# Optimization experiments

Measured on AMD Instinct MI355X. Metric: run time of the kernel, lower is better.

## Reference

```python
import jax, jax.numpy as jnp
import numpy as np

EPS = 1e-5

def layer_norm(x, alpha, beta):
    mean = jnp.mean(x, axis=-1, keepdims=True)
    var = jnp.mean(jnp.square(x - mean), axis=-1, keepdims=True)
    return alpha * ((x - mean) / jnp.sqrt(var + EPS)) + beta

def setup_inputs() -> dict:
    key = jax.random.key(0)
    B, S, D, H = 4, 2048, 1024, 16
    Dff = 4 * D
    ks = jax.random.split(key, 8)
    inp = {
        "x": jax.random.normal(ks[0], (B, S, D), jnp.float32),
        "attention_mask": jnp.ones((B, S), jnp.int32),
        "ln1_alpha": jnp.ones((D,), jnp.float32),
        "ln1_beta": jnp.zeros((D,), jnp.float32),
        "ln2_alpha": jnp.ones((D,), jnp.float32),
        "ln2_beta": jnp.zeros((D,), jnp.float32),
        "Wq": jax.random.normal(ks[1], (D, D), jnp.float32) * 0.05,
        "Wk": jax.random.normal(ks[2], (D, D), jnp.float32) * 0.05,
        "Wv": jax.random.normal(ks[3], (D, D), jnp.float32) * 0.05,
        "Wo": jax.random.normal(ks[4], (D, D), jnp.float32) * 0.05,
        "W1": jax.random.normal(ks[5], (D, Dff), jnp.float32) * 0.02,
        "b1": jnp.zeros((Dff,), jnp.float32),
        "W2": jax.random.normal(ks[6], (Dff, D), jnp.float32) * 0.02,
        "b2": jnp.zeros((D,), jnp.float32),
    }
    return inp

def reference(x, attention_mask, ln1_alpha, ln1_beta, ln2_alpha, ln2_beta,
              Wq, Wk, Wv, Wo, W1, b1, W2, b2):
    B, S, D = x.shape
    H = 16
    dh = D // H

    # LN1 + self-attention
    y = layer_norm(x, ln1_alpha, ln1_beta)
    Q = (y @ Wq).reshape(B, S, H, dh).transpose(0, 2, 1, 3)  # [B,H,S,dh]
    K = (y @ Wk).reshape(B, S, H, dh).transpose(0, 2, 1, 3)
    V = (y @ Wv).reshape(B, S, H, dh).transpose(0, 2, 1, 3)

    scores = jnp.einsum("bhqd,bhkd->bhqk", Q, K) / jnp.sqrt(jnp.float32(dh))
    causal = jnp.tril(jnp.ones((S, S), jnp.float32))  # [S,S]
    tmask = attention_mask.astype(jnp.float32)  # [B,S]
    amask = causal[None, None, :, :] * tmask[:, None, None, :] * tmask[:, None, :, None]
    scores = jnp.where(amask > 0, scores, jnp.float32(-1e30))
    attn = jax.nn.softmax(scores, axis=-1)
    # dropout omitted (deterministic inference)
    ctx = jnp.einsum("bhqk,bhkd->bhqd", attn, V)
    ctx = ctx.transpose(0, 2, 1, 3).reshape(B, S, D)
    x = x + ctx @ Wo

    # LN2 + GELU FFN
    y = layer_norm(x, ln2_alpha, ln2_beta)
    h = jax.nn.gelu(y @ W1 + b1, approximate=False)
    x = x + (h @ W2 + b2)
    return x
```

## Files before the change

### kernel.cpp

```cpp
#include <hip/hip_runtime.h>
#include <math.h>

typedef unsigned short u16;
typedef unsigned int u32;
typedef __attribute__((ext_vector_type(4))) unsigned short u16x4;
typedef __attribute__((ext_vector_type(8))) short bf16x8;
typedef __attribute__((ext_vector_type(4))) float f32x4;

#define B_ 4
#define S_ 2048
#define D_ 1024
#define H_ 16
#define NT (B_*S_)
#define DFF 4096

static __device__ __forceinline__ float bf2f(u16 u) {
    return __uint_as_float(((u32)u) << 16);
}
static __device__ __forceinline__ u16 f2bf(float f) {
    u32 u = __float_as_uint(f);
    u32 r = (u + 0x7fffu + ((u >> 16) & 1u)) >> 16;
    return (u16)r;
}
static __device__ __forceinline__ void gload_lds16(const void* g, void* l) {
    __builtin_amdgcn_global_load_lds(
        (const __attribute__((address_space(1))) void*)g,
        (__attribute__((address_space(3))) void*)l, 16, 0, 0);
}

__global__ void transpose_f2b4(const float* __restrict__ s0, const float* __restrict__ s1,
                               const float* __restrict__ s2, const float* __restrict__ s3,
                               u16* __restrict__ d0, u16* __restrict__ d1,
                               u16* __restrict__ d2, u16* __restrict__ d3,
                               int R, int C) {
    const float* in = s0; u16* out = d0;
    if (blockIdx.z == 1) { in = s1; out = d1; }
    else if (blockIdx.z == 2) { in = s2; out = d2; }
    else if (blockIdx.z == 3) { in = s3; out = d3; }
    __shared__ float t[32][33];
    int c0 = blockIdx.x * 32, r0 = blockIdx.y * 32;
    int x = threadIdx.x, y = threadIdx.y;
    #pragma unroll
    for (int i = 0; i < 4; i++)
        t[y + i*8][x] = in[(long)(r0 + y + i*8) * C + c0 + x];
    __syncthreads();
    #pragma unroll
    for (int i = 0; i < 4; i++)
        out[(long)(c0 + y + i*8) * R + r0 + x] = f2bf(t[x][y + i*8]);
}

__global__ void transpose_f2b(const float* __restrict__ in, u16* __restrict__ out,
                              int R, int C) {
    __shared__ float t[32][33];
    int c0 = blockIdx.x * 32, r0 = blockIdx.y * 32;
    int x = threadIdx.x, y = threadIdx.y;
    #pragma unroll
    for (int i = 0; i < 4; i++)
        t[y + i*8][x] = in[(long)(r0 + y + i*8) * C + c0 + x];
    __syncthreads();
    #pragma unroll
    for (int i = 0; i < 4; i++)
        out[(long)(c0 + y + i*8) * R + r0 + x] = f2bf(t[x][y + i*8]);
}

__global__ void transpose_v(const u16* __restrict__ V, u16* __restrict__ Vt) {
    __shared__ u16 t[32][33];
    int z = blockIdx.z; int b = z >> 4, h = z & 15;
    int s0 = blockIdx.x * 32, d0 = blockIdx.y * 32;
    int x = threadIdx.x, y = threadIdx.y;
    const u16* in = V + ((long)b * S_ + s0) * D_ + h * 64 + d0;
    #pragma unroll
    for (int i = 0; i < 4; i++)
        t[y + i*8][x] = in[(long)(y + i*8) * D_ + x];
    __syncthreads();
    u16* out = Vt + ((long)z * 64 + d0) * S_ + s0;
    #pragma unroll
    for (int i = 0; i < 4; i++)
        out[(long)(y + i*8) * S_ + x] = t[x][y + i*8];
}

__global__ __launch_bounds__(256) void ln_kernel(
    const float* __restrict__ X, const float* __restrict__ alpha,
    const float* __restrict__ beta, u16* __restrict__ Y) {
    int row = blockIdx.x, tid = threadIdx.x;
    float4 xv = ((const float4*)(X + (long)row * D_))[tid];
    float v[4] = {xv.x, xv.y, xv.z, xv.w};
    float s = 0.f, ss = 0.f;
    #pragma unroll
    for (int i = 0; i < 4; i++) { s += v[i]; ss += v[i]*v[i]; }
    #pragma unroll
    for (int off = 32; off >= 1; off >>= 1) {
        s += __shfl_xor(s, off);
        ss += __shfl_xor(ss, off);
    }
    __shared__ float red[8];
    __shared__ float stats[2];
    int w = tid >> 6;
    if ((tid & 63) == 0) { red[w] = s; red[4 + w] = ss; }
    __syncthreads();
    if (tid == 0) {
        float S = red[0] + red[1] + red[2] + red[3];
        float SS = red[4] + red[5] + red[6] + red[7];
        float mean = S * (1.f / D_);
        float var = SS * (1.f / D_) - mean * mean;
        stats[0] = mean; stats[1] = rsqrtf(var + 1e-5f);
    }
    __syncthreads();
    float mean = stats[0], rstd = stats[1];
    float4 av = ((const float4*)alpha)[tid];
    float4 bv = ((const float4*)beta)[tid];
    u16x4 o;
    o[0] = f2bf((v[0] - mean) * rstd * av.x + bv.x);
    o[1] = f2bf((v[1] - mean) * rstd * av.y + bv.y);
    o[2] = f2bf((v[2] - mean) * rstd * av.z + bv.z);
    o[3] = f2bf((v[3] - mean) * rstd * av.w + bv.w);
    *(u16x4*)(Y + (long)row * D_ + tid * 4) = o;
}

#define BM 128
#define BN 128
#define BK 64

__global__ __launch_bounds__(256, 3) void gemm_bt(
    const u16* __restrict__ A,
    const u16* __restrict__ Bt0, const u16* __restrict__ Bt1, const u16* __restrict__ Bt2,
    void* __restrict__ C0, void* __restrict__ C1, void* __restrict__ C2,
    int M, int N, int K, int mode,
    const float* __restrict__ bias, const float* __restrict__ resid) {
    const u16* Bt = Bt0; void* C = C0;
    if (blockIdx.z == 1) { Bt = Bt1; C = C1; }
    else if (blockIdx.z == 2) { Bt = Bt2; C = C2; }

    __shared__ __align__(16) u16 Asm[BM * BK];
    __shared__ __align__(16) u16 Bsm[BN * BK];

    int tid = threadIdx.x;
    int lane = tid & 63, wave = tid >> 6;
    int l15 = lane & 15, quad = lane >> 4;
    int wm = wave & 1, wn = wave >> 1;
    long tm0 = (long)blockIdx.y * BM, tn0 = (long)blockIdx.x * BN;

    int srow = lane >> 3;
    int scol = (lane & 7) * 8;

    f32x4 acc[4][4] = {};

    for (int k0 = 0; k0 < K; k0 += BK) {
        __syncthreads();
        #pragma unroll
        for (int c = 0; c < 4; c++) {
            int chunk = wave * 4 + c;
            int row = chunk * 8 + srow;
            gload_lds16(&A[(tm0 + row) * (long)K + k0 + scol], &Asm[chunk * 512]);
            gload_lds16(&Bt[(tn0 + row) * (long)K + k0 + scol], &Bsm[chunk * 512]);
        }
        __syncthreads();
        #pragma unroll
        for (int ks = 0; ks < 2; ks++) {
            bf16x8 af[4], bfm[4];
            #pragma unroll
            for (int mt = 0; mt < 4; mt++)
                af[mt] = *(const bf16x8*)&Asm[(wm*64 + mt*16 + l15) * BK + ks*32 + quad*8];
            #pragma unroll
            for (int nt = 0; nt < 4; nt++)
                bfm[nt] = *(const bf16x8*)&Bsm[(wn*64 + nt*16 + l15) * BK + ks*32 + quad*8];
            #pragma unroll
            for (int mt = 0; mt < 4; mt++)
                #pragma unroll
                for (int nt = 0; nt < 4; nt++)
                    acc[mt][nt] = __builtin_amdgcn_mfma_f32_16x16x32_bf16(
                        af[mt], bfm[nt], acc[mt][nt], 0, 0, 0);
        }
    }

    #pragma unroll
    for (int mt = 0; mt < 4; mt++) {
        #pragma unroll
        for (int nt = 0; nt < 4; nt++) {
            #pragma unroll
            for (int i = 0; i < 4; i++) {
                long r = tm0 + wm*64 + mt*16 + quad*4 + i;
                long cn = tn0 + wn*64 + nt*16 + l15;
                long idx = r * N + cn;
                float val = acc[mt][nt][i];
                if (mode == 0) {
                    ((u16*)C)[idx] = f2bf(val);
                } else if (mode == 1) {
                    ((float*)C)[idx] = val + resid[idx];
                } else if (mode == 2) {
                    val += bias[cn];
                    val = 0.5f * val * (1.0f + erff(val * 0.70710678118654752f));
                    ((u16*)C)[idx] = f2bf(val);
                } else {
                    ((float*)C)[idx] = val + bias[cn] + resid[idx];
                }
            }
        }
    }
}

#define LDP 72

__global__ __launch_bounds__(256, 2) void attn_kernel(
    const u16* __restrict__ Q, const u16* __restrict__ Kg, const u16* __restrict__ Vt,
    const int* __restrict__ mask, u16* __restrict__ O) {
    __shared__ __align__(16) u16 Psm[4][32 * LDP];
    int tid = threadIdx.x;
    int lane = tid & 63, wave = tid >> 6;
    int l15 = lane & 15, quad = lane >> 4;
    int bh = blockIdx.x; int b = bh >> 4, h = bh & 15;
    int y = blockIdx.y;
    long tokBase = (long)b * S_;
    const float SCL = 0.125f * 1.4426950408889634f;
    const float MMAX = 20.0f;

    const bf16x8 ones = {16256,16256,16256,16256,16256,16256,16256,16256};
    u16* Pw = Psm[wave];
    const int* mb = mask + b * S_;

    int t;
    if (wave == 0)      t = y;
    else if (wave == 1) t = 63 - y;
    else if (wave == 2) t = 31 - y;
    else                t = 32 + y;
    int q0 = t * 32;

    bf16x8 aq[2][2];
    #pragma unroll
    for (int mt = 0; mt < 2; mt++) {
        const u16* qptr = Q + (tokBase + q0 + mt*16 + l15) * D_ + h * 64;
        aq[mt][0] = *(const bf16x8*)(qptr + quad * 8);
        aq[mt][1] = *(const bf16x8*)(qptr + 32 + quad * 8);
    }

    f32x4 o[2][4] = {};
    f32x4 lacc[2] = {};
    int ktiles = t / 2 + 1;

    for (int kt = 0; kt < ktiles; kt++) {
        int k0 = kt * 64;
        bf16x8 kb[4][2], vb[4][2];
        #pragma unroll
        for (int nt = 0; nt < 4; nt++) {
            const u16* kp = Kg + (tokBase + k0 + nt*16 + l15) * D_ + h * 64;
            kb[nt][0] = *(const bf16x8*)(kp + quad * 8);
            kb[nt][1] = *(const bf16x8*)(kp + 32 + quad * 8);
        }
        #pragma unroll
        for (int d = 0; d < 4; d++) {
            const u16* vp = Vt + ((long)bh * 64 + d*16 + l15) * S_ + k0;
            vb[d][0] = *(const bf16x8*)(vp + quad * 8);
            vb[d][1] = *(const bf16x8*)(vp + 32 + quad * 8);
        }

        f32x4 s[2][4] = {};
        #pragma unroll
        for (int nt = 0; nt < 4; nt++) {
            s[0][nt] = __builtin_amdgcn_mfma_f32_16x16x32_bf16(aq[0][0], kb[nt][0], s[0][nt], 0,0,0);
            s[0][nt] = __builtin_amdgcn_mfma_f32_16x16x32_bf16(aq[0][1], kb[nt][1], s[0][nt], 0,0,0);
            s[1][nt] = __builtin_amdgcn_mfma_f32_16x16x32_bf16(aq[1][0], kb[nt][0], s[1][nt], 0,0,0);
            s[1][nt] = __builtin_amdgcn_mfma_f32_16x16x32_bf16(aq[1][1], kb[nt][1], s[1][nt], 0,0,0);
        }

        int mk = 0;
        #pragma unroll
        for (int nt = 0; nt < 4; nt++)
            if (mb[k0 + nt*16 + l15] != 0) mk |= (1 << nt);

        #pragma unroll
        for (int mt = 0; mt < 2; mt++) {
            #pragma unroll
            for (int i = 0; i < 4; i++) {
                int qq = q0 + mt*16 + quad*4 + i;
                #pragma unroll
                for (int nt = 0; nt < 4; nt++) {
                    int kc = k0 + nt*16 + l15;
                    float p = exp2f(fmaf(s[mt][nt][i], SCL, -MMAX));
                    p = (kc <= qq && ((mk >> nt) & 1)) ? p : 0.f;
                    Pw[(mt*16 + quad*4 + i) * LDP + nt*16 + l15] = f2bf(p);
                }
            }
        }
        asm volatile("s_waitcnt lgkmcnt(0)" ::: "memory");

        #pragma unroll
        for (int hv = 0; hv < 2; hv++) {
            bf16x8 ap0 = *(const bf16x8*)&Pw[l15 * LDP + hv*32 + quad*8];
            bf16x8 ap1 = *(const bf16x8*)&Pw[(16 + l15) * LDP + hv*32 + quad*8];
            #pragma unroll
            for (int d = 0; d < 4; d++) {
                o[0][d] = __builtin_amdgcn_mfma_f32_16x16x32_bf16(ap0, vb[d][hv], o[0][d], 0,0,0);
                o[1][d] = __builtin_amdgcn_mfma_f32_16x16x32_bf16(ap1, vb[d][hv], o[1][d], 0,0,0);
            }
            lacc[0] = __builtin_amdgcn_mfma_f32_16x16x32_bf16(ap0, ones, lacc[0], 0,0,0);
            lacc[1] = __builtin_amdgcn_mfma_f32_16x16x32_bf16(ap1, ones, lacc[1], 0,0,0);
        }
    }

    #pragma unroll
    for (int mt = 0; mt < 2; mt++) {
        #pragma unroll
        for (int i = 0; i < 4; i++) {
            float inv = 1.f / lacc[mt][i];
            long r = tokBase + q0 + mt*16 + quad*4 + i;
            #pragma unroll
            for (int d = 0; d < 4; d++)
                O[r * D_ + h*64 + d*16 + l15] = f2bf(o[mt][d][i] * inv);
        }
    }
}

extern "C" void kernel_launch(void* const* d_in, const int* in_sizes, int n_in,
                              void* d_out, int out_size, void* d_ws, size_t ws_size,
                              hipStream_t stream) {
    const float* x    = (const float*)d_in[0];
    const int*   am   = (const int*)d_in[1];
    const float* ln1a = (const float*)d_in[2];
    const float* ln1b = (const float*)d_in[3];
    const float* ln2a = (const float*)d_in[4];
    const float* ln2b = (const float*)d_in[5];
    const float* wq   = (const float*)d_in[6];
    const float* wk   = (const float*)d_in[7];
    const float* wv   = (const float*)d_in[8];
    const float* wo   = (const float*)d_in[9];
    const float* w1   = (const float*)d_in[10];
    const float* b1   = (const float*)d_in[11];
    const float* w2   = (const float*)d_in[12];
    const float* b2   = (const float*)d_in[13];
    float* out = (float*)d_out;

    char* ws = (char*)d_ws;
    const size_t MB16 = (size_t)16 * 1024 * 1024;
    u16* y1      = (u16*)(ws + 0 * MB16);
    u16* q       = (u16*)(ws + 1 * MB16);
    u16* k       = (u16*)(ws + 2 * MB16);
    u16* v       = (u16*)(ws + 3 * MB16);
    u16* wqt     = (u16*)(ws + 4 * MB16 + 0 * (size_t)D_ * D_ * 2);
    u16* wkt     = (u16*)(ws + 4 * MB16 + 1 * (size_t)D_ * D_ * 2);
    u16* wvt     = (u16*)(ws + 4 * MB16 + 2 * (size_t)D_ * D_ * 2);
    u16* wot     = (u16*)(ws + 4 * MB16 + 3 * (size_t)D_ * D_ * 2);
    u16* y2      = y1;
    u16* w1t     = q;
    u16* w2t     = q + (size_t)D_ * DFF;
    u16* h_full  = k;
    u16* ctx     = v;
    u16*   vt  = (u16*)d_out;
    float* x1f = out;

    dim3 tb(32, 8);
    transpose_f2b4<<<dim3(D_/32, D_/32, 4), tb, 0, stream>>>(
        wq, wk, wv, wo, wqt, wkt, wvt, wot, D_, D_);

    ln_kernel<<<NT, 256, 0, stream>>>(x, ln1a, ln1b, y1);

    gemm_bt<<<dim3(D_/BN, NT/BM, 3), 256, 0, stream>>>(
        y1, wqt, wkt, wvt, q, k, v, NT, D_, D_, 0, nullptr, nullptr);

    transpose_v<<<dim3(S_/32, 2, B_*H_), tb, 0, stream>>>(v, vt);

    attn_kernel<<<dim3(B_*H_, 16), 256, 0, stream>>>(q, k, vt, am, ctx);

    gemm_bt<<<dim3(D_/BN, NT/BM, 1), 256, 0, stream>>>(
        ctx, wot, wot, wot, x1f, x1f, x1f, NT, D_, D_, 1, nullptr, x);

    transpose_f2b<<<dim3(DFF/32, D_/32), tb, 0, stream>>>(w1, w1t, D_, DFF);
    transpose_f2b<<<dim3(D_/32, DFF/32), tb, 0, stream>>>(w2, w2t, DFF, D_);

    ln_kernel<<<NT, 256, 0, stream>>>(x1f, ln2a, ln2b, y2);

    gemm_bt<<<dim3(DFF/BN, NT/BM, 1), 256, 0, stream>>>(
        y2, w1t, w1t, w1t, h_full, h_full, h_full, NT, DFF, D_, 2, b1, nullptr);
    gemm_bt<<<dim3(D_/BN, NT/BM, 1), 256, 0, stream>>>(
        h_full, w2t, w2t, w2t, out, out, out, NT, D_, DFF, 3, b2, x1f);
}
```

Baseline: 659.3 us.

## Add 256x256-tile GEMM kernel for QKV and FFN1 with fast tanh GELU

Adds a 512-thread GEMM using 256x256 output tiles and BK=64, and routes the QKV projection and the first FFN projection through it. Larger tiles raise arithmetic intensity and reuse of the LDS-staged operands. The FFN1 epilogue replaces the exact erf GELU with a tanh-approximation built on exp2 and a hardware reciprocal, which cuts epilogue cost but changes numerics slightly. The new kernel has no double buffering, and its large accumulator array may limit occupancy.

```diff
diff --git a/kernel.cpp b/kernel.cpp
--- a/kernel.cpp
+++ b/kernel.cpp
@@ -26,6 +26,13 @@
     __builtin_amdgcn_global_load_lds(
         (const __attribute__((address_space(1))) void*)g,
         (__attribute__((address_space(3))) void*)l, 16, 0, 0);
+}
+static __device__ __forceinline__ float gelu_fast(float x) {
+    float x2 = x * x;
+    float u = x * fmaf(0.044715f, x2, 1.0f);
+    float e = exp2f(2.3022079f * u);
+    float r = __builtin_amdgcn_rcpf(e + 1.0f);
+    return x - x * r;
 }
 
 __global__ void transpose_f2b4(const float* __restrict__ s0, const float* __restrict__ s1,
@@ -193,6 +200,82 @@
                     ((u16*)C)[idx] = f2bf(val);
                 } else {
                     ((float*)C)[idx] = val + bias[cn] + resid[idx];
+                }
+            }
+        }
+    }
+}
+
+#define BM2 256
+#define BN2 256
+#define BK2 64
+
+__global__ __launch_bounds__(512, 2) void gemm256(
+    const u16* __restrict__ A,
+    const u16* __restrict__ Bt0, const u16* __restrict__ Bt1, const u16* __restrict__ Bt2,
+    void* __restrict__ C0, void* __restrict__ C1, void* __restrict__ C2,
+    int M, int N, int K, int mode, const float* __restrict__ bias) {
+    const u16* Bt = Bt0; void* C = C0;
+    if (blockIdx.z == 1) { Bt = Bt1; C = C1; }
+    else if (blockIdx.z == 2) { Bt = Bt2; C = C2; }
+
+    __shared__ __align__(16) u16 Asm[BM2 * BK2];
+    __shared__ __align__(16) u16 Bsm[BN2 * BK2];
+
+    int tid = threadIdx.x;
+    int lane = tid & 63, wave = tid >> 6;
+    int l15 = lane & 15, quad = lane >> 4;
+    int wm = wave & 1, wn = wave >> 1;
+    long tm0 = (long)blockIdx.y * BM2, tn0 = (long)blockIdx.x * BN2;
+
+    int srow = lane >> 3;
+    int scol = (lane & 7) * 8;
+
+    f32x4 acc[8][4] = {};
+
+    for (int k0 = 0; k0 < K; k0 += BK2) {
+        __syncthreads();
+        #pragma unroll
+        for (int c = 0; c < 4; c++) {
+            int chunk = wave * 4 + c;
+            int row = chunk * 8 + srow;
+            gload_lds16(&A[(tm0 + row) * (long)K + k0 + scol], &Asm[chunk * 512]);
+            gload_lds16(&Bt[(tn0 + row) * (long)K + k0 + scol], &Bsm[chunk * 512]);
+        }
+        __syncthreads();
+        #pragma unroll
+        for (int ks = 0; ks < 2; ks++) {
+            bf16x8 af[8], bfm[4];
+            #pragma unroll
+            for (int mt = 0; mt < 8; mt++)
+                af[mt] = *(const bf16x8*)&Asm[(wm*128 + mt*16 + l15) * BK2 + ks*32 + quad*8];
+            #pragma unroll
+            for (int nt = 0; nt < 4; nt++)
+                bfm[nt] = *(const bf16x8*)&Bsm[(wn*64 + nt*16 + l15) * BK2 + ks*32 + quad*8];
+            #pragma unroll
+            for (int mt = 0; mt < 8; mt++)
+                #pragma unroll
+                for (int nt = 0; nt < 4; nt++)
+                    acc[mt][nt] = __builtin_amdgcn_mfma_f32_16x16x32_bf16(
+                        af[mt], bfm[nt], acc[mt][nt], 0, 0, 0);
+        }
+    }
+
+    #pragma unroll
+    for (int mt = 0; mt < 8; mt++) {
+        #pragma unroll
+        for (int nt = 0; nt < 4; nt++) {
+            #pragma unroll
+            for (int i = 0; i < 4; i++) {
+                long r = tm0 + wm*128 + mt*16 + quad*4 + i;
+                long cn = tn0 + wn*64 + nt*16 + l15;
+                long idx = r * N + cn;
+                float val = acc[mt][nt][i];
+                if (mode == 0) {
+                    ((u16*)C)[idx] = f2bf(val);
+                } else {
+                    val += bias[cn];
+                    ((u16*)C)[idx] = f2bf(gelu_fast(val));
                 }
             }
         }
@@ -353,8 +436,8 @@
 
     ln_kernel<<<NT, 256, 0, stream>>>(x, ln1a, ln1b, y1);
 
-    gemm_bt<<<dim3(D_/BN, NT/BM, 3), 256, 0, stream>>>(
-        y1, wqt, wkt, wvt, q, k, v, NT, D_, D_, 0, nullptr, nullptr);
+    gemm256<<<dim3(D_/BN2, NT/BM2, 3), 512, 0, stream>>>(
+        y1, wqt, wkt, wvt, q, k, v, NT, D_, D_, 0, nullptr);
 
     transpose_v<<<dim3(S_/32, 2, B_*H_), tb, 0, stream>>>(v, vt);
 
@@ -368,8 +451,8 @@
 
     ln_kernel<<<NT, 256, 0, stream>>>(x1f, ln2a, ln2b, y2);
 
-    gemm_bt<<<dim3(DFF/BN, NT/BM, 1), 256, 0, stream>>>(
-        y2, w1t, w1t, w1t, h_full, h_full, h_full, NT, DFF, D_, 2, b1, nullptr);
+    gemm256<<<dim3(DFF/BN2, NT/BM2, 1), 512, 0, stream>>>(
+        y2, w1t, w1t, w1t, h_full, h_full, h_full, NT, DFF, D_, 2, b1);
     gemm_bt<<<dim3(D_/BN, NT/BM, 1), 256, 0, stream>>>(
         h_full, w2t, w2t, w2t, out, out, out, NT, D_, DFF, 3, b2, x1f);
 }
```

New measurement: 696.6 us. 5.7% more time.
